# Kernel optimization log

Measured on AMD Instinct MI355X. Metric: run time of the kernel, lower is better.

The kernel has to match this reference:

```python
import jax, jax.numpy as jnp
import numpy as np

EPS = 1e-7  # keras K.epsilon()


def setup_inputs() -> dict:
    key = jax.random.key(0)
    k1, k2, k3, k4 = jax.random.split(key, 4)
    B, T, D, E = 32, 4096, 512, 512
    x = jax.random.normal(k1, (B, T, D), dtype=jnp.float32)
    y = jax.random.normal(k2, (B, E), dtype=jnp.float32)
    W = jax.random.normal(k3, (D, E), dtype=jnp.float32) * (1.0 / np.sqrt(E))
    b = jnp.zeros((1,), dtype=jnp.float32)
    mask = jax.random.randint(k4, (B, T), 0, 2).astype(bool)
    return {"x": x, "y": y, "W": W, "b": b, "mask": mask}


def reference(x, y, W, b, mask):
    # y' = (W @ y^T)^T = y @ W^T  -> [B, D]
    yp = jnp.matmul(y, W.T)
    # broadcast dot-product score over steps: [B, T]
    eij = jnp.einsum('btd,bd->bt', x, yp) + b  # b is (1,), broadcast over T
    a = jnp.exp(jnp.tanh(eij)) * mask.astype(x.dtype)
    a = a / (jnp.sum(a, axis=1, keepdims=True) + EPS)
    return a
```

## Files before the change

### kernel.cpp

```cpp
#include <hip/hip_runtime.h>

#define B_DIM 32
#define T_DIM 4096
#define D_DIM 512
#define E_DIM 512
#define EPS_K 1e-7f

__global__ __launch_bounds__(64) void yp_kernel(const float* __restrict__ y,
                                                const float* __restrict__ W,
                                                float* __restrict__ yp) {
    const int b = blockIdx.x;
    const int d = blockIdx.y * 64 + threadIdx.x;
    __shared__ float ys[E_DIM];
    {
        const float4* src = (const float4*)(y + (size_t)b * E_DIM);
        float4* dst = (float4*)ys;
        dst[threadIdx.x]      = src[threadIdx.x];
        dst[threadIdx.x + 64] = src[threadIdx.x + 64];
    }
    __syncthreads();
    const float* Wr = W + (size_t)d * E_DIM;
    float acc = 0.f;
#pragma unroll 8
    for (int e = 0; e < E_DIM; e += 4) {
        float4 w4 = *(const float4*)(Wr + e);
        acc = fmaf(w4.x, ys[e],     acc);
        acc = fmaf(w4.y, ys[e + 1], acc);
        acc = fmaf(w4.z, ys[e + 2], acc);
        acc = fmaf(w4.w, ys[e + 3], acc);
    }
    yp[(size_t)b * D_DIM + d] = acc;
}

__global__ __launch_bounds__(256) void score_kernel(const float* __restrict__ x,
                                                    const float* __restrict__ yp,
                                                    const float* __restrict__ bias,
                                                    const int* __restrict__ mask,
                                                    float* __restrict__ a_raw) {
    const int b    = blockIdx.y;
    const int wave = threadIdx.x >> 6;
    const int lane = threadIdx.x & 63;
    const int t0   = blockIdx.x * 32 + wave * 8;

    const float4* ypv = (const float4*)(yp + (size_t)b * D_DIM);
    const float4 w0 = ypv[lane];
    const float4 w1 = ypv[lane + 64];
    const float bv = bias[0];

    const size_t xbase = ((size_t)b * T_DIM + (size_t)t0) * D_DIM;
    const float4* xv = (const float4*)(x + xbase);

    for (int i = 0; i < 8; ++i) {
        const float4 x0 = xv[i * (D_DIM / 4) + lane];
        const float4 x1 = xv[i * (D_DIM / 4) + lane + 64];
        float p = x0.x * w0.x + x0.y * w0.y + x0.z * w0.z + x0.w * w0.w
                + x1.x * w1.x + x1.y * w1.y + x1.z * w1.z + x1.w * w1.w;
#pragma unroll
        for (int off = 32; off > 0; off >>= 1) p += __shfl_xor(p, off);
        if (lane == 0) {
            const int t = t0 + i;
            const float s = p + bv;
            const float e = expf(tanhf(s));
            const float a = mask[(size_t)b * T_DIM + t] ? e : 0.f;
            a_raw[(size_t)b * T_DIM + t] = a;
        }
    }
}

__global__ __launch_bounds__(1024) void norm_kernel(const float* __restrict__ a_raw,
                                                    float* __restrict__ out) {
    const int b   = blockIdx.x;
    const int tid = threadIdx.x;
    const float4 v = ((const float4*)(a_raw + (size_t)b * T_DIM))[tid];
    float s = v.x + v.y + v.z + v.w;
#pragma unroll
    for (int off = 32; off > 0; off >>= 1) s += __shfl_xor(s, off);

    __shared__ float wsum[16];
    __shared__ float inv_s;
    const int wave = tid >> 6;
    const int lane = tid & 63;
    if (lane == 0) wsum[wave] = s;
    __syncthreads();
    if (tid == 0) {
        float tot = 0.f;
        for (int i = 0; i < 16; ++i) tot += wsum[i];
        inv_s = 1.0f / (tot + EPS_K);
    }
    __syncthreads();
    const float inv = inv_s;
    const float4 o = make_float4(v.x * inv, v.y * inv, v.z * inv, v.w * inv);
    ((float4*)(out + (size_t)b * T_DIM))[tid] = o;
}

extern "C" void kernel_launch(void* const* d_in, const int* in_sizes, int n_in,
                              void* d_out, int out_size, void* d_ws, size_t ws_size,
                              hipStream_t stream) {
    const float* x    = (const float*)d_in[0];
    const float* y    = (const float*)d_in[1];
    const float* W    = (const float*)d_in[2];
    const float* bias = (const float*)d_in[3];
    const int*   mask = (const int*)d_in[4];
    float* out = (float*)d_out;

    float* yp    = (float*)d_ws;
    float* a_raw = yp + B_DIM * D_DIM;

    yp_kernel<<<dim3(B_DIM, D_DIM / 64), 64, 0, stream>>>(y, W, yp);
    score_kernel<<<dim3(T_DIM / 32, B_DIM), 256, 0, stream>>>(x, yp, bias, mask, a_raw);
    norm_kernel<<<B_DIM, 1024, 0, stream>>>(a_raw, out);
}
```

Baseline: 59.86 us.

## Coalesce W reads in yp kernel and batch x loads in score kernel

The yp kernel changes from one thread per output row, where each thread strides through W, to one wave per output element with coalesced float4 loads and a shuffle reduction, launched as 128x32 blocks of 256 threads. The score kernel now issues all eight rows' x loads up front to expose memory-level parallelism, interleaves the eight shuffle reductions, and computes the eight tanh/exp epilogues in parallel across lanes 0-7 instead of serially in lane 0. This raises register use per thread in exchange for more loads in flight on the bandwidth-bound 256MB x stream.

```diff
diff --git a/kernel.cpp b/kernel.cpp
--- a/kernel.cpp
+++ b/kernel.cpp
@@ -6,30 +6,27 @@
 #define E_DIM 512
 #define EPS_K 1e-7f
 
-__global__ __launch_bounds__(64) void yp_kernel(const float* __restrict__ y,
-                                                const float* __restrict__ W,
-                                                float* __restrict__ yp) {
-    const int b = blockIdx.x;
-    const int d = blockIdx.y * 64 + threadIdx.x;
-    __shared__ float ys[E_DIM];
-    {
-        const float4* src = (const float4*)(y + (size_t)b * E_DIM);
-        float4* dst = (float4*)ys;
-        dst[threadIdx.x]      = src[threadIdx.x];
-        dst[threadIdx.x + 64] = src[threadIdx.x + 64];
-    }
-    __syncthreads();
-    const float* Wr = W + (size_t)d * E_DIM;
-    float acc = 0.f;
-#pragma unroll 8
-    for (int e = 0; e < E_DIM; e += 4) {
-        float4 w4 = *(const float4*)(Wr + e);
-        acc = fmaf(w4.x, ys[e],     acc);
-        acc = fmaf(w4.y, ys[e + 1], acc);
-        acc = fmaf(w4.z, ys[e + 2], acc);
-        acc = fmaf(w4.w, ys[e + 3], acc);
-    }
-    yp[(size_t)b * D_DIM + d] = acc;
+__global__ __launch_bounds__(256) void yp_kernel(const float* __restrict__ y,
+                                                 const float* __restrict__ W,
+                                                 float* __restrict__ yp) {
+    const int b    = blockIdx.y;
+    const int wave = threadIdx.x >> 6;
+    const int lane = threadIdx.x & 63;
+    const int d    = blockIdx.x * 4 + wave;
+
+    const float4* Wv = (const float4*)(W + (size_t)d * E_DIM);
+    const float4* yv = (const float4*)(y + (size_t)b * E_DIM);
+    const float4 w0 = Wv[lane];
+    const float4 w1 = Wv[lane + 64];
+    const float4 y0 = yv[lane];
+    const float4 y1 = yv[lane + 64];
+
+    float p = w0.x * y0.x + w0.y * y0.y + w0.z * y0.z + w0.w * y0.w
+            + w1.x * y1.x + w1.y * y1.y + w1.z * y1.z + w1.w * y1.w;
+#pragma unroll
+    for (int off = 32; off > 0; off >>= 1) p += __shfl_xor(p, off);
+
+    if (lane == 0) yp[(size_t)b * D_DIM + d] = p;
 }
 
 __global__ __launch_bounds__(256) void score_kernel(const float* __restrict__ x,
@@ -45,25 +42,37 @@
     const float4* ypv = (const float4*)(yp + (size_t)b * D_DIM);
     const float4 w0 = ypv[lane];
     const float4 w1 = ypv[lane + 64];
-    const float bv = bias[0];
 
-    const size_t xbase = ((size_t)b * T_DIM + (size_t)t0) * D_DIM;
-    const float4* xv = (const float4*)(x + xbase);
+    const float4* xv = (const float4*)(x + ((size_t)b * T_DIM + (size_t)t0) * D_DIM);
 
+    float4 xa[8], xb[8];
+#pragma unroll
     for (int i = 0; i < 8; ++i) {
-        const float4 x0 = xv[i * (D_DIM / 4) + lane];
-        const float4 x1 = xv[i * (D_DIM / 4) + lane + 64];
-        float p = x0.x * w0.x + x0.y * w0.y + x0.z * w0.z + x0.w * w0.w
-                + x1.x * w1.x + x1.y * w1.y + x1.z * w1.z + x1.w * w1.w;
+        xa[i] = xv[i * (D_DIM / 4) + lane];
+        xb[i] = xv[i * (D_DIM / 4) + lane + 64];
+    }
+
+    float p[8];
 #pragma unroll
-        for (int off = 32; off > 0; off >>= 1) p += __shfl_xor(p, off);
-        if (lane == 0) {
-            const int t = t0 + i;
-            const float s = p + bv;
-            const float e = expf(tanhf(s));
-            const float a = mask[(size_t)b * T_DIM + t] ? e : 0.f;
-            a_raw[(size_t)b * T_DIM + t] = a;
-        }
+    for (int i = 0; i < 8; ++i) {
+        p[i] = xa[i].x * w0.x + xa[i].y * w0.y + xa[i].z * w0.z + xa[i].w * w0.w
+             + xb[i].x * w1.x + xb[i].y * w1.y + xb[i].z * w1.z + xb[i].w * w1.w;
+    }
+
+#pragma unroll
+    for (int off = 32; off > 0; off >>= 1) {
+#pragma unroll
+        for (int i = 0; i < 8; ++i) p[i] += __shfl_xor(p[i], off);
+    }
+
+    if (lane < 8) {
+        float s = (lane == 0) ? p[0] : (lane == 1) ? p[1] : (lane == 2) ? p[2]
+                : (lane == 3) ? p[3] : (lane == 4) ? p[4] : (lane == 5) ? p[5]
+                : (lane == 6) ? p[6] : p[7];
+        const int t = t0 + lane;
+        const float e = expf(tanhf(s + bias[0]));
+        const float a = mask[(size_t)b * T_DIM + t] ? e : 0.f;
+        a_raw[(size_t)b * T_DIM + t] = a;
     }
 }
 
@@ -106,7 +115,7 @@
     float* yp    = (float*)d_ws;
     float* a_raw = yp + B_DIM * D_DIM;
 
-    yp_kernel<<<dim3(B_DIM, D_DIM / 64), 64, 0, stream>>>(y, W, yp);
+    yp_kernel<<<dim3(D_DIM / 4, B_DIM), 256, 0, stream>>>(y, W, yp);
     score_kernel<<<dim3(T_DIM / 32, B_DIM), 256, 0, stream>>>(x, yp, bias, mask, a_raw);
     norm_kernel<<<B_DIM, 1024, 0, stream>>>(a_raw, out);
 }
```

New measurement: 50.81 us. 1.18x faster.
